# Optimization experiments

Measured on AMD Instinct MI355X. Metric: run time of the kernel, lower is better.

## Reference

```python
import jax, jax.numpy as jnp
import numpy as np

D_MODEL = 1024
N_HEADS = 16
D_HEAD = D_MODEL // N_HEADS


def setup_inputs() -> dict:
    key = jax.random.key(0)
    ks = jax.random.split(key, 9)
    s = 1.0 / np.sqrt(D_MODEL)
    x = jax.random.normal(ks[0], (2, 2048, D_MODEL), dtype=jnp.float32)
    Wq = jax.random.uniform(ks[1], (D_MODEL, D_MODEL), jnp.float32, -s, s)
    bq = jax.random.uniform(ks[2], (D_MODEL,), jnp.float32, -s, s)
    Wk = jax.random.uniform(ks[3], (D_MODEL, D_MODEL), jnp.float32, -s, s)
    bk = jax.random.uniform(ks[4], (D_MODEL,), jnp.float32, -s, s)
    Wv = jax.random.uniform(ks[5], (D_MODEL, D_MODEL), jnp.float32, -s, s)
    bv = jax.random.uniform(ks[6], (D_MODEL,), jnp.float32, -s, s)
    Wo = jax.random.uniform(ks[7], (D_MODEL, D_MODEL), jnp.float32, -s, s)
    bo = jax.random.uniform(ks[8], (D_MODEL,), jnp.float32, -s, s)
    return {"x": x, "Wq": Wq, "bq": bq, "Wk": Wk, "bk": bk,
            "Wv": Wv, "bv": bv, "Wo": Wo, "bo": bo}


def reference(x, Wq, bq, Wk, bk, Wv, bv, Wo, bo):
    B, T, _ = x.shape
    # projections: (B, T, d_model) -> (B, H, T, d_head)
    def split_heads(y):
        return y.reshape(B, T, N_HEADS, D_HEAD).transpose(0, 2, 1, 3)
    Q = split_heads(x @ Wq + bq)
    K = split_heads(x @ Wk + bk)
    V = split_heads(x @ Wv + bv)
    scores = jnp.einsum('bhqd,bhkd->bhqk', Q, K) / jnp.sqrt(jnp.float32(D_HEAD))
    causal = jnp.tril(jnp.ones((T, T), dtype=bool))  # allowed positions
    scores = jnp.where(causal, scores, -jnp.inf)
    attn = jax.nn.softmax(scores, axis=-1)
    out = jnp.einsum('bhqk,bhkd->bhqd', attn, V)
    out = out.transpose(0, 2, 1, 3).reshape(B, T, D_MODEL)
    return out @ Wo + bo
```

## Files before the change

### kernel.cpp

```cpp
#include <hip/hip_runtime.h>

typedef unsigned short u16;
typedef unsigned int u32;

#define DM 1024
#define NH 16
#define DH 64
#define BB 2
#define TT 2048

#define SCLQ 0.18033688f

using frag8  = __attribute__((ext_vector_type(8))) short;
using bf16x8 = __attribute__((ext_vector_type(8))) __bf16;
using f32x4  = __attribute__((ext_vector_type(4))) float;

__device__ inline u16 f2bf(float f) {
  union { float f; u32 u; } v; v.f = f;
  u32 r = v.u + 0x7fffu + ((v.u >> 16) & 1u);
  return (u16)(r >> 16);
}

__device__ inline f32x4 mfma_bf16(frag8 a, frag8 b, f32x4 c) {
  return __builtin_amdgcn_mfma_f32_16x16x32_bf16(
      __builtin_bit_cast(bf16x8, a), __builtin_bit_cast(bf16x8, b), c, 0, 0, 0);
}

__device__ inline void gld16(void* lds, const void* g) {
  __builtin_amdgcn_global_load_lds(
      (const __attribute__((address_space(1))) void*)g,
      (__attribute__((address_space(3))) void*)lds, 16, 0, 0);
}

__device__ inline int swi(int row, int chunk) {
  return row * 64 + ((chunk ^ (row & 7)) << 3);
}

__device__ inline int sidx128(int row, int col) {
  return row * 128 + ((((col >> 3) ^ (row & 7)) << 3) | (col & 7));
}

__global__ __launch_bounds__(256) void cvt_x_kernel(const float* __restrict__ X,
                                                    u16* __restrict__ Y) {
  int i = blockIdx.x * 256 + threadIdx.x;
  float4 v = ((const float4*)X)[i];
  ushort4 o;
  o.x = f2bf(v.x); o.y = f2bf(v.y); o.z = f2bf(v.z); o.w = f2bf(v.w);
  ((ushort4*)Y)[i] = o;
}

__global__ __launch_bounds__(256) void transpose_w_kernel(
    const float* __restrict__ W0, const float* __restrict__ W1,
    const float* __restrict__ W2, const float* __restrict__ W3,
    u16* __restrict__ O0, u16* __restrict__ O1,
    u16* __restrict__ O2, u16* __restrict__ O3) {
  const float* W; u16* Ot;
  switch (blockIdx.z) {
    case 0: W = W0; Ot = O0; break;
    case 1: W = W1; Ot = O1; break;
    case 2: W = W2; Ot = O2; break;
    default: W = W3; Ot = O3; break;
  }
  __shared__ u16 Ls[64][72];
  int tid = threadIdx.x;
  int n0 = blockIdx.x * 64;
  int k0 = blockIdx.y * 64;
#pragma unroll
  for (int p = 0; p < 4; ++p) {
    int id = tid + p * 256;
    int row = id >> 4;
    int c4 = (id & 15) * 4;
    float4 v = *(const float4*)&W[(size_t)(k0 + row) * DM + n0 + c4];
    ushort4 o; o.x = f2bf(v.x); o.y = f2bf(v.y); o.z = f2bf(v.z); o.w = f2bf(v.w);
    *(ushort4*)&Ls[row][c4] = o;
  }
  __syncthreads();
#pragma unroll
  for (int p = 0; p < 4; ++p) {
    int id = tid + p * 256;
    int row = id >> 4;
    int c4 = (id & 15) * 4;
    ushort4 o;
    o.x = Ls[c4 + 0][row]; o.y = Ls[c4 + 1][row];
    o.z = Ls[c4 + 2][row]; o.w = Ls[c4 + 3][row];
    *(ushort4*)&Ot[(size_t)(n0 + row) * DM + k0 + c4] = o;
  }
}

__global__ __launch_bounds__(256, 3) void gemm_qkv_kernel(
    const u16* __restrict__ A, const u16* __restrict__ Bt,
    const float* __restrict__ b0, const float* __restrict__ b1,
    const float* __restrict__ b2,
    u16* __restrict__ QK, u16* __restrict__ Vt) {
  constexpr int K = 1024;
  __shared__ u16 sm[16384];
  u16* As = sm;
  u16* Bs = sm + 8192;
  int tid = threadIdx.x;
  int lane = tid & 63, w = tid >> 6;
  int qd = lane >> 4, ln = lane & 15;
  int wm = (w & 1) * 64, wn = (w >> 1) * 64;
  int lin = blockIdx.y * 24 + blockIdx.x;
  int xcd = lin & 7, j = lin >> 3;
  int m_idx = ((xcd >> 1) << 3) | (j & 7);
  int n_idx = (xcd & 1) * 12 + (j >> 3);
  int m0 = m_idx * 128, n0 = n_idx * 128;
  f32x4 z = {0.f, 0.f, 0.f, 0.f};
  f32x4 acc[4][4];
#pragma unroll
  for (int mi = 0; mi < 4; ++mi)
#pragma unroll
    for (int ni = 0; ni < 4; ++ni) acc[mi][ni] = z;

  const u16* ga = A + (size_t)(m0 + w * 32 + (lane >> 2)) * K + (lane & 3) * 8;
  const u16* gb = Bt + (size_t)(n0 + w * 32 + (lane >> 2)) * K + (lane & 3) * 8;

  gld16(&As[w * 1024],       ga);
  gld16(&As[w * 1024 + 512], ga + 16 * K);
  gld16(&Bs[w * 1024],       gb);
  gld16(&Bs[w * 1024 + 512], gb + 16 * K);

  for (int k0 = 0; k0 < K; k0 += 32) {
    int cur = (k0 >> 5) & 1;
    __syncthreads();
    if (k0 + 32 < K) {
      int nb = cur ^ 1;
      gld16(&As[nb * 4096 + w * 1024],       ga + k0 + 32);
      gld16(&As[nb * 4096 + w * 1024 + 512], ga + k0 + 32 + 16 * K);
      gld16(&Bs[nb * 4096 + w * 1024],       gb + k0 + 32);
      gld16(&Bs[nb * 4096 + w * 1024 + 512], gb + k0 + 32 + 16 * K);
    }
    frag8 af[4], bfr[4];
#pragma unroll
    for (int mi = 0; mi < 4; ++mi)
      af[mi] = *(const frag8*)&As[cur * 4096 + (wm + mi * 16 + ln) * 32 + qd * 8];
#pragma unroll
    for (int ni = 0; ni < 4; ++ni)
      bfr[ni] = *(const frag8*)&Bs[cur * 4096 + (wn + ni * 16 + ln) * 32 + qd * 8];
#pragma unroll
    for (int mi = 0; mi < 4; ++mi)
#pragma unroll
      for (int ni = 0; ni < 4; ++ni)
        acc[mi][ni] = mfma_bf16(af[mi], bfr[ni], acc[mi][ni]);
  }

  __syncthreads();

  if (n0 < 2048) {
    bool isq = (n0 < 1024);
#pragma unroll
    for (int ni = 0; ni < 4; ++ni) {
      int c_loc = wn + ni * 16 + ln;
      int col = n0 + c_loc;
      float bias = isq ? b0[col] : b1[col - 1024];
#pragma unroll
      for (int mi = 0; mi < 4; ++mi) {
        int rbase = wm + mi * 16 + qd * 4;
#pragma unroll
        for (int r = 0; r < 4; ++r) {
          float v = acc[mi][ni][r] + bias;
          if (isq) v *= SCLQ;
          sm[sidx128(rbase + r, c_loc)] = f2bf(v);
        }
      }
    }
    __syncthreads();
#pragma unroll
    for (int p = 0; p < 8; ++p) {
      int id = p * 256 + tid;
      int tr = id >> 4, cr = id & 15;
      uint4 v = *(const uint4*)&sm[tr * 128 + ((cr ^ (tr & 7)) << 3)];
      *(uint4*)&QK[(size_t)(m0 + tr) * 2048 + n0 + cr * 8] = v;
    }
  } else {
    int b = m0 >> 11, tb = m0 & 2047;
    int n0v = n0 - 2048;
#pragma unroll
    for (int ni = 0; ni < 4; ++ni) {
      int c_loc = wn + ni * 16 + ln;
      float bias = b2[n0v + c_loc];
#pragma unroll
      for (int mi = 0; mi < 4; ++mi) {
        int tbase = wm + mi * 16 + qd * 4;
        u32 lo = ((u32)f2bf(acc[mi][ni][1] + bias) << 16) | f2bf(acc[mi][ni][0] + bias);
        u32 hi = ((u32)f2bf(acc[mi][ni][3] + bias) << 16) | f2bf(acc[mi][ni][2] + bias);
        uint2 pk; pk.x = lo; pk.y = hi;
        int idx = c_loc * 128 + ((((tbase >> 3) ^ (c_loc & 7)) << 3) | (tbase & 7));
        *(uint2*)&sm[idx] = pk;
      }
    }
    __syncthreads();
#pragma unroll
    for (int p = 0; p < 8; ++p) {
      int id = p * 256 + tid;
      int d_loc = id >> 4, tc = id & 15;
      uint4 v = *(const uint4*)&sm[d_loc * 128 + ((tc ^ (d_loc & 7)) << 3)];
      *(uint4*)&Vt[(size_t)(b * 1024 + n0v + d_loc) * 2048 + tb + tc * 8] = v;
    }
  }
}

__global__ __launch_bounds__(256) void gemm_out_kernel(
    const u16* __restrict__ A, const u16* __restrict__ Bt,
    const float* __restrict__ b0, float* __restrict__ Cf) {
  constexpr int K = 1024;
  __shared__ u16 As[2][4096];
  __shared__ u16 Bs[2][2048];
  int tid = threadIdx.x;
  int lane = tid & 63, w = tid >> 6;
  int qd = lane >> 4, ln = lane & 15;
  int lin = blockIdx.y * 16 + blockIdx.x;
  int xcd = lin & 7, j = lin >> 3;
  int m_idx = ((xcd >> 1) << 3) | (j & 7);
  int n_idx = ((xcd & 1) << 3) | (j >> 3);
  int m0 = m_idx * 128, n0 = n_idx * 64;
  f32x4 z = {0.f, 0.f, 0.f, 0.f};
  f32x4 acc[2][4];
#pragma unroll
  for (int mi = 0; mi < 2; ++mi)
#pragma unroll
    for (int ni = 0; ni < 4; ++ni) acc[mi][ni] = z;

  const u16* ga = A + (size_t)(m0 + w * 32 + (lane >> 2)) * K + (lane & 3) * 8;
  const u16* gb = Bt + (size_t)(n0 + w * 16 + (lane >> 2)) * K + (lane & 3) * 8;

  gld16(&As[0][w * 1024],       ga);
  gld16(&As[0][w * 1024 + 512], ga + 16 * K);
  gld16(&Bs[0][w * 512],        gb);

  for (int k0 = 0; k0 < K; k0 += 32) {
    int cur = (k0 >> 5) & 1;
    __syncthreads();
    if (k0 + 32 < K) {
      int nb = cur ^ 1;
      gld16(&As[nb][w * 1024],       ga + k0 + 32);
      gld16(&As[nb][w * 1024 + 512], ga + k0 + 32 + 16 * K);
      gld16(&Bs[nb][w * 512],        gb + k0 + 32);
    }
    frag8 af[2], bfr[4];
#pragma unroll
    for (int mi = 0; mi < 2; ++mi)
      af[mi] = *(const frag8*)&As[cur][(w * 32 + mi * 16 + ln) * 32 + qd * 8];
#pragma unroll
    for (int ni = 0; ni < 4; ++ni)
      bfr[ni] = *(const frag8*)&Bs[cur][(ni * 16 + ln) * 32 + qd * 8];
#pragma unroll
    for (int mi = 0; mi < 2; ++mi)
#pragma unroll
      for (int ni = 0; ni < 4; ++ni)
        acc[mi][ni] = mfma_bf16(af[mi], bfr[ni], acc[mi][ni]);
  }

#pragma unroll
  for (int ni = 0; ni < 4; ++ni) {
    int col = n0 + ni * 16 + ln;
    float bias = b0[col];
#pragma unroll
    for (int mi = 0; mi < 2; ++mi) {
      int row = m0 + w * 32 + mi * 16 + qd * 4;
#pragma unroll
      for (int r = 0; r < 4; ++r)
        Cf[(size_t)(row + r) * 1024 + col] = acc[mi][ni][r] + bias;
    }
  }
}

__global__ __launch_bounds__(256, 4) void flash7_kernel(const u16* __restrict__ QK,
                                                        const u16* __restrict__ Vt,
                                                        u16* __restrict__ O) {
  int lin = blockIdx.y * 32 + blockIdx.x;
  int xcd = lin & 7, u = lin >> 3;
  int a = u & 31, r = u >> 5;
  int bh = (xcd << 2) | r;
  int qt = (r & 1) ? (31 - a) : a;
  int b = bh >> 4, h = bh & 15;
  int q0 = qt * 64;
  __shared__ u16 Ks[2 * 4096];
  __shared__ u16 Vs[2 * 4096];
  __shared__ u16 Ps[4096];
  int tid = threadIdx.x;
  int lane = tid & 63, w = tid >> 6;
  int qd = lane >> 4, ln = lane & 15;

  frag8 qf[2];
#pragma unroll
  for (int kk = 0; kk < 2; ++kk)
    qf[kk] = *(const frag8*)&QK[(size_t)(b * TT + q0 + w * 16 + ln) * 2048 +
                                h * 64 + kk * 32 + qd * 8];

  int lr = lane >> 3, lc = (lane & 7) ^ lr;
  const u16* Kg  = &QK[(size_t)(b * TT + w * 16 + lr) * 2048 + 1024 + h * 64 + lc * 8];
  const u16* Kg2 = Kg + 8 * 2048;
  const u16* Vg  = &Vt[(size_t)(bh * 64 + w * 16 + lr) * 2048 + lc * 8];
  const u16* Vg2 = Vg + 8 * 2048;
  int ldsw = w * 1024;

  int nkt = qt + 1;

  gld16(&Ks[ldsw],       Kg);
  gld16(&Ks[ldsw + 512], Kg2);
  gld16(&Vs[ldsw],       Vg);
  gld16(&Vs[ldsw + 512], Vg2);

  float l = 0.f;
  f32x4 z = {0.f, 0.f, 0.f, 0.f};
  f32x4 o[4] = {z, z, z, z};

  for (int kt = 0; kt < nkt; ++kt) {
    int cur = kt & 1;
    int cb = cur * 4096;
    __syncthreads();

    if (kt + 1 < nkt) {
      int nb = (cur ^ 1) * 4096;
      size_t ko = (size_t)(kt + 1) * 64 * 2048;
      int vo = (kt + 1) * 64;
      gld16(&Ks[nb + ldsw],       Kg + ko);
      gld16(&Ks[nb + ldsw + 512], Kg2 + ko);
      gld16(&Vs[nb + ldsw],       Vg + vo);
      gld16(&Vs[nb + ldsw + 512], Vg2 + vo);
    }

    bool diag = (kt == qt);

    f32x4 s[4] = {z, z, z, z};
    __builtin_amdgcn_s_setprio(1);
#pragma unroll
    for (int mi = 0; mi < 4; ++mi) {
      if (diag && mi > w) continue;
#pragma unroll
      for (int kk = 0; kk < 2; ++kk) {
        frag8 ak = *(const frag8*)&Ks[cb + swi(mi * 16 + ln, 4 * kk + qd)];
        s[mi] = mfma_bf16(ak, qf[kk], s[mi]);
      }
    }
    __builtin_amdgcn_s_setprio(0);

#pragma unroll
    for (int mi = 0; mi < 4; ++mi) {
      int pb = swi(w * 16 + ln, 2 * mi + (qd >> 1)) + (qd & 1) * 4;
      if (diag && mi > w) {
        uint2 zz; zz.x = 0u; zz.y = 0u;
        *(uint2*)&Ps[pb] = zz;
        continue;
      }
      float p0 = __builtin_amdgcn_exp2f(s[mi][0]);
      float p1 = __builtin_amdgcn_exp2f(s[mi][1]);
      float p2 = __builtin_amdgcn_exp2f(s[mi][2]);
      float p3 = __builtin_amdgcn_exp2f(s[mi][3]);
      if (diag && mi == w) {
        p0 = (qd * 4 + 0 <= ln) ? p0 : 0.f;
        p1 = (qd * 4 + 1 <= ln) ? p1 : 0.f;
        p2 = (qd * 4 + 2 <= ln) ? p2 : 0.f;
        p3 = (qd * 4 + 3 <= ln) ? p3 : 0.f;
      }
      l += (p0 + p1) + (p2 + p3);
      u32 u0 = __builtin_bit_cast(u32, p0) + 0x8000u;
      u32 u1 = __builtin_bit_cast(u32, p1) + 0x8000u;
      u32 u2 = __builtin_bit_cast(u32, p2) + 0x8000u;
      u32 u3 = __builtin_bit_cast(u32, p3) + 0x8000u;
      uint2 pk;
      pk.x = __builtin_amdgcn_perm(u1, u0, 0x07060302u);
      pk.y = __builtin_amdgcn_perm(u3, u2, 0x07060302u);
      *(uint2*)&Ps[pb] = pk;
    }

    __builtin_amdgcn_s_setprio(1);
#pragma unroll
    for (int kk = 0; kk < 2; ++kk) {
      if (diag && kk == 1 && w < 2) continue;
      frag8 bp = *(const frag8*)&Ps[swi(w * 16 + ln, 4 * kk + qd)];
#pragma unroll
      for (int mi = 0; mi < 4; ++mi) {
        frag8 av = *(const frag8*)&Vs[cb + swi(mi * 16 + ln, 4 * kk + qd)];
        o[mi] = mfma_bf16(av, bp, o[mi]);
      }
    }
    __builtin_amdgcn_s_setprio(0);
  }

  l += __shfl_xor(l, 16);
  l += __shfl_xor(l, 32);
  float rl = 1.0f / l;

#pragma unroll
  for (int mi = 0; mi < 4; ++mi) {
    ushort4 ov;
    ov.x = f2bf(o[mi][0] * rl); ov.y = f2bf(o[mi][1] * rl);
    ov.z = f2bf(o[mi][2] * rl); ov.w = f2bf(o[mi][3] * rl);
    *(ushort4*)&O[(size_t)(b * TT + q0 + w * 16 + ln) * DM + h * 64 + mi * 16 + qd * 4] = ov;
  }
}

extern "C" void kernel_launch(void* const* d_in, const int* in_sizes, int n_in,
                              void* d_out, int out_size, void* d_ws, size_t ws_size,
                              hipStream_t stream) {
  const float* x  = (const float*)d_in[0];
  const float* Wq = (const float*)d_in[1];
  const float* bq = (const float*)d_in[2];
  const float* Wk = (const float*)d_in[3];
  const float* bk = (const float*)d_in[4];
  const float* Wv = (const float*)d_in[5];
  const float* bv = (const float*)d_in[6];
  const float* Wo = (const float*)d_in[7];
  const float* bo = (const float*)d_in[8];

  char* ws = (char*)d_ws;
  const size_t MB = 1ull << 20;
  u16* xbf  = (u16*)(ws + 0);
  u16* Wcat = (u16*)(ws + 8 * MB);
  u16* Wot  = (u16*)(ws + 14 * MB);
  u16* QKb  = (u16*)(ws + 16 * MB);
  u16* Vtb  = (u16*)(ws + 40 * MB);
  u16* Ob   = (u16*)(ws + 48 * MB);

  cvt_x_kernel<<<4096, 256, 0, stream>>>(x, xbf);
  transpose_w_kernel<<<dim3(16, 16, 4), 256, 0, stream>>>(
      Wq, Wk, Wv, Wo, Wcat, Wcat + 1024 * 1024, Wcat + 2 * 1024 * 1024, Wot);
  gemm_qkv_kernel<<<dim3(24, 32), 256, 0, stream>>>(
      xbf, Wcat, bq, bk, bv, QKb, Vtb);
  flash7_kernel<<<dim3(32, 32), 256, 0, stream>>>(QKb, Vtb, Ob);
  gemm_out_kernel<<<dim3(16, 32), 256, 0, stream>>>(Ob, Wot, bo, (float*)d_out);
}
```

Baseline: 179.1 us.

## Triple-buffer GEMM k-loop with explicit vmcnt waits and MFMA priority

Both projection GEMM kernels switch from double-buffered LDS staging to a three-stage ring, prefetching two k-tiles ahead. Partial s_waitcnt vmcnt counts plus a raw s_barrier let a wave wait only for the tile it is about to use, not for every outstanding load. s_setprio is raised around the MFMA block so matrix issue is favoured. The aim is to hide global-load latency better, at the cost of more LDS per block (48KB for QKV), which may lower occupancy.

```diff
diff --git a/kernel.cpp b/kernel.cpp
--- a/kernel.cpp
+++ b/kernel.cpp
@@ -93,9 +93,8 @@
     const float* __restrict__ b2,
     u16* __restrict__ QK, u16* __restrict__ Vt) {
   constexpr int K = 1024;
-  __shared__ u16 sm[16384];
-  u16* As = sm;
-  u16* Bs = sm + 8192;
+  constexpr int NT = 32;
+  __shared__ u16 sm[24576];
   int tid = threadIdx.x;
   int lane = tid & 63, w = tid >> 6;
   int qd = lane >> 4, ln = lane & 15;
@@ -115,33 +114,48 @@
   const u16* ga = A + (size_t)(m0 + w * 32 + (lane >> 2)) * K + (lane & 3) * 8;
   const u16* gb = Bt + (size_t)(n0 + w * 32 + (lane >> 2)) * K + (lane & 3) * 8;
 
-  gld16(&As[w * 1024],       ga);
-  gld16(&As[w * 1024 + 512], ga + 16 * K);
-  gld16(&Bs[w * 1024],       gb);
-  gld16(&Bs[w * 1024 + 512], gb + 16 * K);
-
-  for (int k0 = 0; k0 < K; k0 += 32) {
-    int cur = (k0 >> 5) & 1;
-    __syncthreads();
-    if (k0 + 32 < K) {
-      int nb = cur ^ 1;
-      gld16(&As[nb * 4096 + w * 1024],       ga + k0 + 32);
-      gld16(&As[nb * 4096 + w * 1024 + 512], ga + k0 + 32 + 16 * K);
-      gld16(&Bs[nb * 4096 + w * 1024],       gb + k0 + 32);
-      gld16(&Bs[nb * 4096 + w * 1024 + 512], gb + k0 + 32 + 16 * K);
-    }
+  auto stage = [&](int t, int buf) {
+    u16* Ab = sm + buf * 4096;
+    u16* Bb = sm + 12288 + buf * 4096;
+    gld16(&Ab[w * 1024],       ga + t * 32);
+    gld16(&Ab[w * 1024 + 512], ga + t * 32 + 16 * K);
+    gld16(&Bb[w * 1024],       gb + t * 32);
+    gld16(&Bb[w * 1024 + 512], gb + t * 32 + 16 * K);
+  };
+
+  stage(0, 0);
+  stage(1, 1);
+
+  int cur = 0, nbuf = 2;
+  for (int t = 0; t < NT; ++t) {
+    if (t < NT - 1) {
+      asm volatile("s_waitcnt vmcnt(4)" ::: "memory");
+    } else {
+      asm volatile("s_waitcnt vmcnt(0)" ::: "memory");
+    }
+    __builtin_amdgcn_sched_barrier(0);
+    __builtin_amdgcn_s_barrier();
+    if (t + 2 < NT) {
+      stage(t + 2, nbuf);
+      nbuf = (nbuf == 2) ? 0 : nbuf + 1;
+    }
+    const u16* Ab = sm + cur * 4096;
+    const u16* Bb = sm + 12288 + cur * 4096;
     frag8 af[4], bfr[4];
 #pragma unroll
     for (int mi = 0; mi < 4; ++mi)
-      af[mi] = *(const frag8*)&As[cur * 4096 + (wm + mi * 16 + ln) * 32 + qd * 8];
+      af[mi] = *(const frag8*)&Ab[(wm + mi * 16 + ln) * 32 + qd * 8];
 #pragma unroll
     for (int ni = 0; ni < 4; ++ni)
-      bfr[ni] = *(const frag8*)&Bs[cur * 4096 + (wn + ni * 16 + ln) * 32 + qd * 8];
+      bfr[ni] = *(const frag8*)&Bb[(wn + ni * 16 + ln) * 32 + qd * 8];
+    __builtin_amdgcn_s_setprio(1);
 #pragma unroll
     for (int mi = 0; mi < 4; ++mi)
 #pragma unroll
       for (int ni = 0; ni < 4; ++ni)
         acc[mi][ni] = mfma_bf16(af[mi], bfr[ni], acc[mi][ni]);
+    __builtin_amdgcn_s_setprio(0);
+    cur = (cur == 2) ? 0 : cur + 1;
   }
 
   __syncthreads();
@@ -204,8 +218,8 @@
     const u16* __restrict__ A, const u16* __restrict__ Bt,
     const float* __restrict__ b0, float* __restrict__ Cf) {
   constexpr int K = 1024;
-  __shared__ u16 As[2][4096];
-  __shared__ u16 Bs[2][2048];
+  constexpr int NT = 32;
+  __shared__ u16 sm[18432];
   int tid = threadIdx.x;
   int lane = tid & 63, w = tid >> 6;
   int qd = lane >> 4, ln = lane & 15;
@@ -224,31 +238,47 @@
   const u16* ga = A + (size_t)(m0 + w * 32 + (lane >> 2)) * K + (lane & 3) * 8;
   const u16* gb = Bt + (size_t)(n0 + w * 16 + (lane >> 2)) * K + (lane & 3) * 8;
 
-  gld16(&As[0][w * 1024],       ga);
-  gld16(&As[0][w * 1024 + 512], ga + 16 * K);
-  gld16(&Bs[0][w * 512],        gb);
-
-  for (int k0 = 0; k0 < K; k0 += 32) {
-    int cur = (k0 >> 5) & 1;
-    __syncthreads();
-    if (k0 + 32 < K) {
-      int nb = cur ^ 1;
-      gld16(&As[nb][w * 1024],       ga + k0 + 32);
-      gld16(&As[nb][w * 1024 + 512], ga + k0 + 32 + 16 * K);
-      gld16(&Bs[nb][w * 512],        gb + k0 + 32);
-    }
+  auto stage = [&](int t, int buf) {
+    u16* Ab = sm + buf * 4096;
+    u16* Bb = sm + 12288 + buf * 2048;
+    gld16(&Ab[w * 1024],       ga + t * 32);
+    gld16(&Ab[w * 1024 + 512], ga + t * 32 + 16 * K);
+    gld16(&Bb[w * 512],        gb + t * 32);
+  };
+
+  stage(0, 0);
+  stage(1, 1);
+
+  int cur = 0, nbuf = 2;
+  for (int t = 0; t < NT; ++t) {
+    if (t < NT - 1) {
+      asm volatile("s_waitcnt vmcnt(3)" ::: "memory");
+    } else {
+      asm volatile("s_waitcnt vmcnt(0)" ::: "memory");
+    }
+    __builtin_amdgcn_sched_barrier(0);
+    __builtin_amdgcn_s_barrier();
+    if (t + 2 < NT) {
+      stage(t + 2, nbuf);
+      nbuf = (nbuf == 2) ? 0 : nbuf + 1;
+    }
+    const u16* Ab = sm + cur * 4096;
+    const u16* Bb = sm + 12288 + cur * 2048;
     frag8 af[2], bfr[4];
 #pragma unroll
     for (int mi = 0; mi < 2; ++mi)
-      af[mi] = *(const frag8*)&As[cur][(w * 32 + mi * 16 + ln) * 32 + qd * 8];
+      af[mi] = *(const frag8*)&Ab[(w * 32 + mi * 16 + ln) * 32 + qd * 8];
 #pragma unroll
     for (int ni = 0; ni < 4; ++ni)
-      bfr[ni] = *(const frag8*)&Bs[cur][(ni * 16 + ln) * 32 + qd * 8];
+      bfr[ni] = *(const frag8*)&Bb[(ni * 16 + ln) * 32 + qd * 8];
+    __builtin_amdgcn_s_setprio(1);
 #pragma unroll
     for (int mi = 0; mi < 2; ++mi)
 #pragma unroll
       for (int ni = 0; ni < 4; ++ni)
         acc[mi][ni] = mfma_bf16(af[mi], bfr[ni], acc[mi][ni]);
+    __builtin_amdgcn_s_setprio(0);
+    cur = (cur == 2) ? 0 : cur + 1;
   }
 
 #pragma unroll
```

After: 176.5 us. About the same (-1.5%).
